# Optimization experiments

Measured on AMD Instinct MI355X. Metric: run time of the kernel, lower is better.

Reference implementation:

```python
import jax, jax.numpy as jnp
import numpy as np
import math

DILATION_RATES = (1, 2, 4, 8)


def setup_inputs() -> dict:
    key = jax.random.key(0)
    B, S, D = 2, 2048, 512
    R = len(DILATION_RATES)
    ks = jax.random.split(key, 8)
    s = 0.02  # init scale
    x = jax.random.normal(ks[0], (B, S, D), dtype=jnp.float32)
    Wq = jax.random.normal(ks[1], (D, D), dtype=jnp.float32) * s
    Wk = jax.random.normal(ks[2], (D, D), dtype=jnp.float32) * s
    Wv = jax.random.normal(ks[3], (D, D), dtype=jnp.float32) * s
    Wr = jax.random.normal(ks[4], (R, D, D), dtype=jnp.float32) * s  # per-rate projections
    Wo = jax.random.normal(ks[5], (R * D, D), dtype=jnp.float32) * s
    bq = jnp.zeros((D,), jnp.float32)
    bk = jnp.zeros((D,), jnp.float32)
    bv = jnp.zeros((D,), jnp.float32)
    br = jnp.zeros((R, D), jnp.float32)
    bo = jnp.zeros((D,), jnp.float32)
    return {"x": x, "Wq": Wq, "bq": bq, "Wk": Wk, "bk": bk, "Wv": Wv, "bv": bv,
            "Wr": Wr, "br": br, "Wo": Wo, "bo": bo}


def reference(x, Wq, bq, Wk, bk, Wv, bv, Wr, br, Wo, bo):
    B, S, D = x.shape
    Q = x @ Wq + bq
    K = x @ Wk + bk
    V = x @ Wv + bv
    # Dense scores are identical across rates in the original (recomputed each loop);
    # compute once for the same math.
    scores = jnp.einsum('bid,bjd->bij', Q, K) / math.sqrt(D)  # [B,S,S]
    idx = jnp.arange(S)
    outs, attns = [], []
    for r, rate in enumerate(DILATION_RATES):
        # mask[i, j] = 1 iff (j % rate == 0) and (j <= i)
        mask = (idx[None, :] % rate == 0) & (idx[None, :] <= idx[:, None])  # [S,S]
        sc = jnp.where(mask[None, :, :], scores, jnp.float32(-1e9))
        attn = jax.nn.softmax(sc, axis=-1)  # dropout is identity at eval
        attns.append(attn)
        ctx = jnp.einsum('bij,bjd->bid', attn, V)
        outs.append(ctx @ Wr[r] + br[r])
    combined = jnp.concatenate(outs, axis=-1)  # [B,S,4D]
    output = combined @ Wo + bo  # [B,S,D]
    avg_attention = jnp.mean(jnp.stack(attns, axis=0), axis=0)  # [B,S,S]
    return output, avg_attention
```

## Files before the change

### kernel.cpp

```cpp
#include <hip/hip_runtime.h>
#include <hip/hip_bf16.h>
#include <math.h>

#define B_ 2
#define S_ 2048
#define D_ 512
#define R_ 4
#define KP 3840

typedef __attribute__((ext_vector_type(8))) __bf16 bf16x8;
typedef __attribute__((ext_vector_type(4))) float f32x4;

enum { M_QKV = 0, M_SCORES = 1, M_WEFFT = 2, M_W2T = 3, M_PF = 4 };

__device__ __forceinline__ void g2l16(const void* gp, void* lp) {
    __builtin_amdgcn_global_load_lds(
        (const __attribute__((address_space(1))) unsigned int*)(unsigned long long)gp,
        (__attribute__((address_space(3))) unsigned int*)(unsigned int)(unsigned long long)lp,
        16, 0, 0);
}

template<int MODE, int TBM, int TBN>
__device__ __forceinline__ void mfma_body(
    int bx, int by, int bz,
    const short* __restrict__ A, const short* __restrict__ B,
    const float* __restrict__ bias, void* __restrict__ Cv,
    int lda, int ldb, int ldc, int K,
    long strA, long strB, long strC, long strBias, float scale,
    __bf16* sAt, __bf16* sBt)
{
    constexpr int WM = TBM / 2, WN = TBN / 2;
    constexpr int FM = WM / 16, FN = WN / 16;

    const int tid  = threadIdx.x;
    const int lane = tid & 63, wid = tid >> 6;
    const int ln15 = lane & 15, quad = lane >> 4;
    const int wy = wid & 1, wx = wid >> 1;

    const int col0 = bx * TBN;
    const int row0 = by * TBM;
    const int z    = bz;

    if constexpr (MODE == M_SCORES) {
        if (col0 > row0 + TBM - 1) return;
    }

    const short* Ab = A + (size_t)z * strA;
    const short* Bb = B + (size_t)z * strB;
    const float* biasb = bias + (size_t)z * strBias;

    int rate = 1, seg = 0;
    if constexpr (MODE == M_W2T) {
        int rIdx;
        if      (col0 >= 3584) { rate = 8; seg = 3584; rIdx = 3; }
        else if (col0 >= 3072) { rate = 4; seg = 3072; rIdx = 2; }
        else if (col0 >= 2048) { rate = 2; seg = 2048; rIdx = 1; }
        else                   { rate = 1; seg = 0;    rIdx = 0; }
        Ab += (size_t)rIdx * D_ * D_;
    }

    f32x4 acc[FM][FN];
    #pragma unroll
    for (int u = 0; u < FM; ++u)
        #pragma unroll
        for (int v = 0; v < FN; ++v)
            acc[u][v] = (f32x4){0.f, 0.f, 0.f, 0.f};

    for (int k0 = 0; k0 < K; k0 += 128) {
        if constexpr (MODE == M_PF) {
            int kr, ks;
            if      (k0 >= 3584) { kr = 8; ks = 3584; }
            else if (k0 >= 3072) { kr = 4; ks = 3072; }
            else if (k0 >= 2048) { kr = 2; ks = 2048; }
            else                 { kr = 1; ks = 0;    }
            if ((k0 - ks) * kr > row0 + TBM - 1) continue;
        }

        #pragma unroll
        for (int t = 0; t < TBM * 16; t += 256) {
            int idx = t + tid;
            int r = idx >> 4, clog = (idx & 15) ^ (r & 7);
            const short* g = Ab + (size_t)(row0 + r) * lda + k0 + clog * 8;
            g2l16(g, (char*)sAt + (t + wid * 64) * 16);
        }
        #pragma unroll
        for (int t = 0; t < TBN * 16; t += 256) {
            int idx = t + tid;
            int r = idx >> 4, clog = (idx & 15) ^ (r & 7);
            int grow;
            if constexpr (MODE == M_W2T) grow = (col0 + r - seg) * rate;
            else                         grow = col0 + r;
            const short* g = Bb + (size_t)grow * ldb + k0 + clog * 8;
            g2l16(g, (char*)sBt + (t + wid * 64) * 16);
        }
        __syncthreads();

        #pragma unroll
        for (int kk = 0; kk < 128; kk += 32) {
            bf16x8 af[FM], bfr[FN];
            #pragma unroll
            for (int u = 0; u < FM; ++u) {
                int ra = wy * WM + u * 16 + ln15;
                int ch = (kk >> 3) + quad;
                af[u] = *(const bf16x8*)&sAt[ra * 128 + (ch ^ (ra & 7)) * 8];
            }
            #pragma unroll
            for (int v = 0; v < FN; ++v) {
                int rb = wx * WN + v * 16 + ln15;
                int ch = (kk >> 3) + quad;
                bfr[v] = *(const bf16x8*)&sBt[rb * 128 + (ch ^ (rb & 7)) * 8];
            }
            #pragma unroll
            for (int u = 0; u < FM; ++u)
                #pragma unroll
                for (int v = 0; v < FN; ++v)
                    acc[u][v] = __builtin_amdgcn_mfma_f32_16x16x32_bf16(
                        af[u], bfr[v], acc[u][v], 0, 0, 0);
        }
        __syncthreads();
    }

    constexpr bool OUTBF = (MODE != M_PF);
    #pragma unroll
    for (int u = 0; u < FM; ++u) {
        int rg = row0 + wy * WM + u * 16 + quad * 4;
        #pragma unroll
        for (int v = 0; v < FN; ++v) {
            int cg = col0 + wx * WN + v * 16 + ln15;
            float bv = 0.f;
            if constexpr (MODE == M_QKV || MODE == M_PF) bv = biasb[cg];
            #pragma unroll
            for (int rr = 0; rr < 4; ++rr) {
                float val = acc[u][v][rr];
                if constexpr (MODE == M_SCORES) val *= scale;
                val += bv;
                if constexpr (OUTBF)
                    ((__hip_bfloat16*)Cv)[(size_t)z * strC + (size_t)(rg + rr) * ldc + cg] =
                        __float2bfloat16(val);
                else
                    ((float*)Cv)[(size_t)z * strC + (size_t)(rg + rr) * ldc + cg] = val;
            }
        }
    }
}

__global__ __launch_bounds__(256) void prep_all(
    const float* __restrict__ x,  const float* __restrict__ Wr,
    const float* __restrict__ Wq, const float* __restrict__ Wk,
    const float* __restrict__ Wv, const float* __restrict__ Wo,
    const float* __restrict__ bq, const float* __restrict__ bk,
    const float* __restrict__ bv, const float* __restrict__ br,
    __hip_bfloat16* __restrict__ xb,  __hip_bfloat16* __restrict__ Wrb,
    __hip_bfloat16* __restrict__ WqT, __hip_bfloat16* __restrict__ WoT,
    float* __restrict__ biasqkv, float* __restrict__ beff_part)
{
    __shared__ float tsh[32][33];
    const int f = blockIdx.x, tid = threadIdx.x;

    if (f < 3072) {
        const float* in; __hip_bfloat16* out; size_t off;
        if (f < 2048) { in = x;  out = xb;  off = ((size_t)f * 256 + tid) * 4; }
        else          { in = Wr; out = Wrb; off = ((size_t)(f - 2048) * 256 + tid) * 4; }
        float4 v = *(const float4*)(in + off);
        out[off + 0] = __float2bfloat16(v.x);
        out[off + 1] = __float2bfloat16(v.y);
        out[off + 2] = __float2bfloat16(v.z);
        out[off + 3] = __float2bfloat16(v.w);
    } else if (f < 4864) {
        int g = f - 3072;
        int cx = g & 15, y = g >> 4;
        const float* in; __hip_bfloat16* out; int Rr, r0;
        if (y < 48) {
            int w = y >> 4;
            in = (w == 0) ? Wq : (w == 1) ? Wk : Wv;
            out = WqT + (size_t)w * 512 * 512;
            Rr = 512; r0 = (y & 15) * 32;
        } else {
            in = Wo; out = WoT; Rr = 2048; r0 = (y - 48) * 32;
        }
        int c0 = cx * 32;
        int tx = tid & 31, ty = tid >> 5;
        #pragma unroll
        for (int dy = 0; dy < 32; dy += 8)
            tsh[ty + dy][tx] = in[(size_t)(r0 + ty + dy) * 512 + c0 + tx];
        __syncthreads();
        #pragma unroll
        for (int dy = 0; dy < 32; dy += 8)
            out[(size_t)(c0 + ty + dy) * Rr + r0 + tx] = __float2bfloat16(tsh[tx][ty + dy]);
    } else if (f < 4880) {
        int j = f - 4864, m0 = j * 128;
        float a0 = 0.f, a1 = 0.f;
        for (int m = m0; m < m0 + 128; ++m) {
            float b = br[m];
            a0 += b * Wo[(size_t)m * D_ + tid];
            a1 += b * Wo[(size_t)m * D_ + tid + 256];
        }
        beff_part[j * 512 + tid]       = a0;
        beff_part[j * 512 + tid + 256] = a1;
    } else {
        for (int k = tid; k < 512; k += 256) {
            biasqkv[k]        = bq[k];
            biasqkv[512 + k]  = bk[k];
            biasqkv[1024 + k] = bv[k];
        }
    }
}

__global__ __launch_bounds__(256) void k_qkv_wefft(
    const short* __restrict__ xb, const short* __restrict__ WqT,
    const float* __restrict__ biasqkv, short* __restrict__ Qb,
    const short* __restrict__ WoT, const short* __restrict__ Wrb,
    short* __restrict__ WeffT,
    const float* __restrict__ beff_part, const float* __restrict__ bo,
    float* __restrict__ beff)
{
    __shared__ __bf16 sA[64 * 128];
    __shared__ __bf16 sB[128 * 128];
    int f = blockIdx.x;
    if (f < 768) {
        mfma_body<M_QKV, 64, 128>(f & 3, (f >> 2) & 63, f >> 8,
            xb, WqT, biasqkv, Qb, 512, 512, 512, 512,
            0, 512L * 512, (long)B_ * S_ * D_, 512, 0.f, sA, sB);
    } else if (f < 896) {
        int g = f - 768;
        mfma_body<M_WEFFT, 64, 128>(g & 3, (g >> 2) & 7, g >> 5,
            WoT, Wrb, beff, WeffT, 2048, 512, 512, 512,
            512, (long)D_ * D_, (long)D_ * D_, 0, 0.f, sA, sB);
    } else {
        int t = threadIdx.x;
        for (int n = t; n < 512; n += 256) {
            float a = bo[n];
            #pragma unroll
            for (int j = 0; j < 16; ++j) a += beff_part[j * 512 + n];
            beff[n] = a;
        }
    }
}

__global__ __launch_bounds__(256) void k_scores_w2t(
    const short* __restrict__ Qb, const short* __restrict__ Kb,
    short* __restrict__ P, const short* __restrict__ WeffT,
    const short* __restrict__ Vb, short* __restrict__ W2T,
    const float* __restrict__ dummy, float scale)
{
    __shared__ __bf16 sA[64 * 128];
    __shared__ __bf16 sB[128 * 128];
    int f = blockIdx.x;
    if (f < 1024) {
        mfma_body<M_SCORES, 64, 128>(f & 15, (f >> 4) & 31, f >> 9,
            Qb, Kb, dummy, P, 512, 512, KP, 512,
            (long)S_ * D_, (long)S_ * D_, (long)S_ * KP, 0, scale, sA, sB);
    } else {
        int g = f - 1024;
        mfma_body<M_W2T, 64, 128>(g % 30, (g / 30) & 7, g / 240,
            WeffT, Vb, dummy, W2T, 512, 512, KP, 512,
            0, (long)S_ * D_, 512L * KP, 0, 0.f, sA, sB);
    }
}

__global__ __launch_bounds__(256) void k_pf(
    const short* __restrict__ P, const short* __restrict__ W2T,
    const float* __restrict__ beff, float* __restrict__ out)
{
    __shared__ __bf16 sA[64 * 128];
    __shared__ __bf16 sB[64 * 128];
    mfma_body<M_PF, 64, 64>(blockIdx.x, gridDim.y - 1 - blockIdx.y, blockIdx.z,
        P, W2T, beff, out, KP, KP, 512, KP,
        (long)S_ * KP, 512L * KP, (long)S_ * D_, 0, 0.f, sA, sB);
}

__global__ __launch_bounds__(256) void softmax_p(float* __restrict__ avg_out,
                                                 __hip_bfloat16* __restrict__ P)
{
    __shared__ float s_p[S_];
    __shared__ float red[4];
    __shared__ float bs[8];

    int i   = blockIdx.x;
    int b   = blockIdx.y;
    int tid = threadIdx.x;
    int wv  = tid >> 6;
    int ln  = tid & 63;

    __bf16* prow = (__bf16*)P + ((size_t)b * S_ + i) * KP;

    const int cnt1 = i + 1;
    const int nchL = (cnt1 + 7) >> 3;
    const int n4   = cnt1 >> 2;

    float m = -INFINITY;
    for (int t = tid; t < nchL; t += 256) {
        bf16x8 v = ((const bf16x8*)prow)[t];
        int base = t << 3;
        #pragma unroll
        for (int k = 0; k < 8; ++k) {
            float xv = (base + k < cnt1) ? (float)v[k] : -INFINITY;
            s_p[base + k] = xv;
            m = fmaxf(m, xv);
        }
    }
    #pragma unroll
    for (int o = 32; o > 0; o >>= 1) m = fmaxf(m, __shfl_xor(m, o, 64));
    if (ln == 0) red[wv] = m;
    if (tid < 8) bs[tid] = 0.f;
    __syncthreads();
    m = fmaxf(fmaxf(red[0], red[1]), fmaxf(red[2], red[3]));

    float a0 = 0.f, a1 = 0.f, a2 = 0.f, a3 = 0.f;
    for (int t = tid; t < n4; t += 256) {
        float4 v = ((float4*)s_p)[t];
        v.x = __expf(v.x - m); v.y = __expf(v.y - m);
        v.z = __expf(v.z - m); v.w = __expf(v.w - m);
        ((float4*)s_p)[t] = v;
        a0 += v.x; a1 += v.y; a2 += v.z; a3 += v.w;
    }
    for (int j = (n4 << 2) + tid; j < cnt1; j += 256) {
        float e = __expf(s_p[j] - m); s_p[j] = e;
        atomicAdd(&bs[j & 7], e);
    }
    float o0 = __shfl_xor(a0, 1, 64), o1 = __shfl_xor(a1, 1, 64);
    float o2 = __shfl_xor(a2, 1, 64), o3 = __shfl_xor(a3, 1, 64);
    float b8[8];
    if ((ln & 1) == 0) {
        b8[0]=a0; b8[1]=a1; b8[2]=a2; b8[3]=a3; b8[4]=o0; b8[5]=o1; b8[6]=o2; b8[7]=o3;
    } else {
        b8[0]=o0; b8[1]=o1; b8[2]=o2; b8[3]=o3; b8[4]=a0; b8[5]=a1; b8[6]=a2; b8[7]=a3;
    }
    #pragma unroll
    for (int st = 2; st < 64; st <<= 1)
        #pragma unroll
        for (int k = 0; k < 8; ++k) b8[k] += __shfl_xor(b8[k], st, 64);
    if (ln == 0) {
        #pragma unroll
        for (int k = 0; k < 8; ++k) atomicAdd(&bs[k], b8[k]);
    }
    __syncthreads();

    float S1 = bs[0]+bs[1]+bs[2]+bs[3]+bs[4]+bs[5]+bs[6]+bs[7];
    float S2 = bs[0]+bs[2]+bs[4]+bs[6];
    float S4 = bs[0]+bs[4];
    float S8 = bs[0];
    float i1 = 1.f/S1, i2 = 1.f/S2, i4 = 1.f/S4, i8 = 1.f/S8;
    float c0 = 0.25f*(i1+i2+i4+i8), c1 = 0.25f*i1, c2 = 0.25f*(i1+i2);
    float c4 = 0.25f*(i1+i2+i4);
    float cA[4] = {c0, c1, c2, c1};
    float cB[4] = {c4, c1, c2, c1};

    float* arow = avg_out + ((size_t)b * S_ + i) * S_;
    for (int t = tid; t < S_ / 4; t += 256) {
        int j = t << 2;
        float4 e = ((float4*)s_p)[t];
        const float* cc = (t & 1) ? cB : cA;
        float4 o;
        o.x = (j     < cnt1) ? e.x * cc[0] : 0.f;
        o.y = (j + 1 < cnt1) ? e.y * cc[1] : 0.f;
        o.z = (j + 2 < cnt1) ? e.z * cc[2] : 0.f;
        o.w = (j + 3 < cnt1) ? e.w * cc[3] : 0.f;
        ((float4*)arow)[t] = o;
    }

    const float invSr[4]  = {i1, i2, i4, i8};
    const int   segoff[4] = {0, 2048, 3072, 3584};
    const int   imax = i | 63;
    #pragma unroll
    for (int ri = 0; ri < 4; ++ri) {
        int seg    = segoff[ri];
        int segLen = S_ >> ri;
        int cnt    = (i >> ri) + 1;
        int tlim   = min(segLen, ((imax >> ri) & ~127) + 128);
        float invS = invSr[ri];
        int nch = tlim >> 3;
        for (int t8 = tid; t8 < nch; t8 += 256) {
            int t0 = t8 << 3;
            bf16x8 w;
            #pragma unroll
            for (int k = 0; k < 8; ++k) {
                int t = t0 + k;
                float p = (t < cnt) ? s_p[t << ri] * invS : 0.f;
                w[k] = (__bf16)p;
            }
            *((bf16x8*)(prow + seg) + t8) = w;
        }
    }
}

extern "C" void kernel_launch(void* const* d_in, const int* in_sizes, int n_in,
                              void* d_out, int out_size, void* d_ws, size_t ws_size,
                              hipStream_t stream)
{
    const float* x  = (const float*)d_in[0];
    const float* Wq = (const float*)d_in[1];
    const float* bq = (const float*)d_in[2];
    const float* Wk = (const float*)d_in[3];
    const float* bk = (const float*)d_in[4];
    const float* Wv = (const float*)d_in[5];
    const float* bv = (const float*)d_in[6];
    const float* Wr = (const float*)d_in[7];
    const float* br = (const float*)d_in[8];
    const float* Wo = (const float*)d_in[9];
    const float* bo = (const float*)d_in[10];

    float* out = (float*)d_out;
    float* avg = out + (size_t)B_ * S_ * D_;

    char* wsb = (char*)d_ws;
    short* xb  = (short*)(wsb);
    short* Qb  = (short*)(wsb + (4u  << 20));
    short* Vb  = (short*)(wsb + (12u << 20));
    short* P   = (short*)(wsb + (16u << 20));
    short* W2T = (short*)(wsb + (16u << 20) + 31457280u);
    short* WqT = W2T;
    short* Wrb   = (short*)((char*)W2T + 7864320u);
    short* WoT   = (short*)((char*)Wrb + 2097152u);
    short* WeffT = (short*)((char*)WoT + 2097152u);
    float* beff      = (float*)((char*)WeffT + 2097152u);
    float* biasqkv   = beff + 512;
    float* beff_part = biasqkv + 1536;

    const float scale = (float)(1.0 / sqrt((double)D_));

    prep_all<<<dim3(4881), 256, 0, stream>>>(
        x, Wr, Wq, Wk, Wv, Wo, bq, bk, bv, br,
        (__hip_bfloat16*)xb, (__hip_bfloat16*)Wrb,
        (__hip_bfloat16*)WqT, (__hip_bfloat16*)WoT, biasqkv, beff_part);

    k_qkv_wefft<<<dim3(897), 256, 0, stream>>>(
        xb, WqT, biasqkv, Qb, WoT, Wrb, WeffT, beff_part, bo, beff);

    k_scores_w2t<<<dim3(1504), 256, 0, stream>>>(
        Qb, Qb + (size_t)B_ * S_ * D_, P, WeffT, Vb, W2T, beff, scale);

    softmax_p<<<dim3(S_, B_), 256, 0, stream>>>(avg, (__hip_bfloat16*)P);

    k_pf<<<dim3(8, 32, 2), 256, 0, stream>>>(P, W2T, beff, out);
}
```

Before: 212.6 us.

## Enlarge GEMM M-tiles to 128 and restructure softmax with presplit dilation buffers

Raises the M tile of the QKV, Weff, scores and W2T GEMMs from 64 to 128 rows and halves their grids, so each block reuses its loaded B tile across more rows. The softmax kernel also changes. It drops the row-max pass and applies exp directly to the raw scores, relying on the scores being small. It writes strided copies of the exponentials into separate shared-memory arrays per dilation rate, so the bf16 writeback reads them contiguously, and it replaces the shared atomics with per-wave partial sums. The exp without a max shift risks overflow on other inputs, and the larger tiles use more shared memory while launching fewer blocks.

```diff
diff --git a/kernel.cpp b/kernel.cpp
--- a/kernel.cpp
+++ b/kernel.cpp
@@ -214,16 +214,16 @@
     const float* __restrict__ beff_part, const float* __restrict__ bo,
     float* __restrict__ beff)
 {
-    __shared__ __bf16 sA[64 * 128];
+    __shared__ __bf16 sA[128 * 128];
     __shared__ __bf16 sB[128 * 128];
     int f = blockIdx.x;
-    if (f < 768) {
-        mfma_body<M_QKV, 64, 128>(f & 3, (f >> 2) & 63, f >> 8,
+    if (f < 384) {
+        mfma_body<M_QKV, 128, 128>(f & 3, (f >> 2) & 31, f >> 7,
             xb, WqT, biasqkv, Qb, 512, 512, 512, 512,
             0, 512L * 512, (long)B_ * S_ * D_, 512, 0.f, sA, sB);
-    } else if (f < 896) {
-        int g = f - 768;
-        mfma_body<M_WEFFT, 64, 128>(g & 3, (g >> 2) & 7, g >> 5,
+    } else if (f < 448) {
+        int g = f - 384;
+        mfma_body<M_WEFFT, 128, 128>(g & 3, (g >> 2) & 3, g >> 4,
             WoT, Wrb, beff, WeffT, 2048, 512, 512, 512,
             512, (long)D_ * D_, (long)D_ * D_, 0, 0.f, sA, sB);
     } else {
@@ -243,16 +243,16 @@
     const short* __restrict__ Vb, short* __restrict__ W2T,
     const float* __restrict__ dummy, float scale)
 {
-    __shared__ __bf16 sA[64 * 128];
+    __shared__ __bf16 sA[128 * 128];
     __shared__ __bf16 sB[128 * 128];
     int f = blockIdx.x;
-    if (f < 1024) {
-        mfma_body<M_SCORES, 64, 128>(f & 15, (f >> 4) & 31, f >> 9,
+    if (f < 512) {
+        mfma_body<M_SCORES, 128, 128>(f & 15, (f >> 4) & 15, f >> 8,
             Qb, Kb, dummy, P, 512, 512, KP, 512,
             (long)S_ * D_, (long)S_ * D_, (long)S_ * KP, 0, scale, sA, sB);
     } else {
-        int g = f - 1024;
-        mfma_body<M_W2T, 64, 128>(g % 30, (g / 30) & 7, g / 240,
+        int g = f - 512;
+        mfma_body<M_W2T, 128, 128>(g % 30, (g / 30) & 3, g / 120,
             WeffT, Vb, dummy, W2T, 512, 512, KP, 512,
             0, (long)S_ * D_, 512L * KP, 0, 0.f, sA, sB);
     }
@@ -272,9 +272,11 @@
 __global__ __launch_bounds__(256) void softmax_p(float* __restrict__ avg_out,
                                                  __hip_bfloat16* __restrict__ P)
 {
-    __shared__ float s_p[S_];
-    __shared__ float red[4];
-    __shared__ float bs[8];
+    __shared__ float s_e[S_];
+    __shared__ float s_d2[S_ / 2];
+    __shared__ float s_d4[S_ / 4];
+    __shared__ float s_d8[S_ / 8];
+    __shared__ float wsum[4][8];
 
     int i   = blockIdx.x;
     int b   = blockIdx.y;
@@ -283,63 +285,49 @@
     int ln  = tid & 63;
 
     __bf16* prow = (__bf16*)P + ((size_t)b * S_ + i) * KP;
-
     const int cnt1 = i + 1;
-    const int nchL = (cnt1 + 7) >> 3;
-    const int n4   = cnt1 >> 2;
-
-    float m = -INFINITY;
-    for (int t = tid; t < nchL; t += 256) {
+    const int nch  = (cnt1 + 7) >> 3;
+
+    for (int t = tid; t < S_ / 4; t += 256) ((float4*)s_e)[t] = (float4){0, 0, 0, 0};
+    for (int t = tid; t < S_ / 8; t += 256) ((float4*)s_d2)[t] = (float4){0, 0, 0, 0};
+    if (tid < S_ / 16) ((float4*)s_d4)[tid] = (float4){0, 0, 0, 0};
+    if (tid < S_ / 32) ((float4*)s_d8)[tid] = (float4){0, 0, 0, 0};
+    __syncthreads();
+
+    float a[8] = {0.f, 0.f, 0.f, 0.f, 0.f, 0.f, 0.f, 0.f};
+    for (int t = tid; t < nch; t += 256) {
         bf16x8 v = ((const bf16x8*)prow)[t];
         int base = t << 3;
+        float e[8];
         #pragma unroll
         for (int k = 0; k < 8; ++k) {
-            float xv = (base + k < cnt1) ? (float)v[k] : -INFINITY;
-            s_p[base + k] = xv;
-            m = fmaxf(m, xv);
-        }
+            float ev = (base + k < cnt1) ? __expf((float)v[k]) : 0.f;
+            e[k] = ev;
+            a[k] += ev;
+        }
+        ((float4*)s_e)[2 * t]     = (float4){e[0], e[1], e[2], e[3]};
+        ((float4*)s_e)[2 * t + 1] = (float4){e[4], e[5], e[6], e[7]};
+        ((float4*)s_d2)[t]        = (float4){e[0], e[2], e[4], e[6]};
+        ((float2*)s_d4)[t]        = (float2){e[0], e[4]};
+        s_d8[t]                   = e[0];
     }
     #pragma unroll
-    for (int o = 32; o > 0; o >>= 1) m = fmaxf(m, __shfl_xor(m, o, 64));
-    if (ln == 0) red[wv] = m;
-    if (tid < 8) bs[tid] = 0.f;
+    for (int st = 1; st < 64; st <<= 1)
+        #pragma unroll
+        for (int k = 0; k < 8; ++k) a[k] += __shfl_xor(a[k], st, 64);
+    if (ln == 0)
+        #pragma unroll
+        for (int k = 0; k < 8; ++k) wsum[wv][k] = a[k];
     __syncthreads();
-    m = fmaxf(fmaxf(red[0], red[1]), fmaxf(red[2], red[3]));
-
-    float a0 = 0.f, a1 = 0.f, a2 = 0.f, a3 = 0.f;
-    for (int t = tid; t < n4; t += 256) {
-        float4 v = ((float4*)s_p)[t];
-        v.x = __expf(v.x - m); v.y = __expf(v.y - m);
-        v.z = __expf(v.z - m); v.w = __expf(v.w - m);
-        ((float4*)s_p)[t] = v;
-        a0 += v.x; a1 += v.y; a2 += v.z; a3 += v.w;
-    }
-    for (int j = (n4 << 2) + tid; j < cnt1; j += 256) {
-        float e = __expf(s_p[j] - m); s_p[j] = e;
-        atomicAdd(&bs[j & 7], e);
-    }
-    float o0 = __shfl_xor(a0, 1, 64), o1 = __shfl_xor(a1, 1, 64);
-    float o2 = __shfl_xor(a2, 1, 64), o3 = __shfl_xor(a3, 1, 64);
-    float b8[8];
-    if ((ln & 1) == 0) {
-        b8[0]=a0; b8[1]=a1; b8[2]=a2; b8[3]=a3; b8[4]=o0; b8[5]=o1; b8[6]=o2; b8[7]=o3;
-    } else {
-        b8[0]=o0; b8[1]=o1; b8[2]=o2; b8[3]=o3; b8[4]=a0; b8[5]=a1; b8[6]=a2; b8[7]=a3;
-    }
+
+    float bsum[8];
     #pragma unroll
-    for (int st = 2; st < 64; st <<= 1)
-        #pragma unroll
-        for (int k = 0; k < 8; ++k) b8[k] += __shfl_xor(b8[k], st, 64);
-    if (ln == 0) {
-        #pragma unroll
-        for (int k = 0; k < 8; ++k) atomicAdd(&bs[k], b8[k]);
-    }
-    __syncthreads();
-
-    float S1 = bs[0]+bs[1]+bs[2]+bs[3]+bs[4]+bs[5]+bs[6]+bs[7];
-    float S2 = bs[0]+bs[2]+bs[4]+bs[6];
-    float S4 = bs[0]+bs[4];
-    float S8 = bs[0];
+    for (int k = 0; k < 8; ++k)
+        bsum[k] = wsum[0][k] + wsum[1][k] + wsum[2][k] + wsum[3][k];
+    float S1 = bsum[0]+bsum[1]+bsum[2]+bsum[3]+bsum[4]+bsum[5]+bsum[6]+bsum[7];
+    float S2 = bsum[0]+bsum[2]+bsum[4]+bsum[6];
+    float S4 = bsum[0]+bsum[4];
+    float S8 = bsum[0];
     float i1 = 1.f/S1, i2 = 1.f/S2, i4 = 1.f/S4, i8 = 1.f/S8;
     float c0 = 0.25f*(i1+i2+i4+i8), c1 = 0.25f*i1, c2 = 0.25f*(i1+i2);
     float c4 = 0.25f*(i1+i2+i4);
@@ -348,38 +336,31 @@
 
     float* arow = avg_out + ((size_t)b * S_ + i) * S_;
     for (int t = tid; t < S_ / 4; t += 256) {
-        int j = t << 2;
-        float4 e = ((float4*)s_p)[t];
+        float4 e = ((float4*)s_e)[t];
         const float* cc = (t & 1) ? cB : cA;
-        float4 o;
-        o.x = (j     < cnt1) ? e.x * cc[0] : 0.f;
-        o.y = (j + 1 < cnt1) ? e.y * cc[1] : 0.f;
-        o.z = (j + 2 < cnt1) ? e.z * cc[2] : 0.f;
-        o.w = (j + 3 < cnt1) ? e.w * cc[3] : 0.f;
-        ((float4*)arow)[t] = o;
-    }
-
-    const float invSr[4]  = {i1, i2, i4, i8};
-    const int   segoff[4] = {0, 2048, 3072, 3584};
-    const int   imax = i | 63;
+        ((float4*)arow)[t] = (float4){e.x*cc[0], e.y*cc[1], e.z*cc[2], e.w*cc[3]};
+    }
+
+    const float* srcs[4] = {s_e, s_d2, s_d4, s_d8};
+    const float invSr[4] = {i1, i2, i4, i8};
+    const int segoff[4]  = {0, 2048, 3072, 3584};
+    const int imax = i | 63;
     #pragma unroll
     for (int ri = 0; ri < 4; ++ri) {
-        int seg    = segoff[ri];
-        int segLen = S_ >> ri;
-        int cnt    = (i >> ri) + 1;
-        int tlim   = min(segLen, ((imax >> ri) & ~127) + 128);
+        const float* src = srcs[ri];
         float invS = invSr[ri];
-        int nch = tlim >> 3;
-        for (int t8 = tid; t8 < nch; t8 += 256) {
-            int t0 = t8 << 3;
+        int tlim = min(S_ >> ri, ((imax >> ri) & ~127) + 128);
+        int nch8 = tlim >> 3;
+        __bf16* dst = prow + segoff[ri];
+        for (int t8 = tid; t8 < nch8; t8 += 256) {
+            float4 lo = ((const float4*)src)[2 * t8];
+            float4 hi = ((const float4*)src)[2 * t8 + 1];
             bf16x8 w;
-            #pragma unroll
-            for (int k = 0; k < 8; ++k) {
-                int t = t0 + k;
-                float p = (t < cnt) ? s_p[t << ri] * invS : 0.f;
-                w[k] = (__bf16)p;
-            }
-            *((bf16x8*)(prow + seg) + t8) = w;
+            w[0] = (__bf16)(lo.x * invS); w[1] = (__bf16)(lo.y * invS);
+            w[2] = (__bf16)(lo.z * invS); w[3] = (__bf16)(lo.w * invS);
+            w[4] = (__bf16)(hi.x * invS); w[5] = (__bf16)(hi.y * invS);
+            w[6] = (__bf16)(hi.z * invS); w[7] = (__bf16)(hi.w * invS);
+            ((bf16x8*)dst)[t8] = w;
         }
     }
 }
@@ -424,10 +405,10 @@
         (__hip_bfloat16*)xb, (__hip_bfloat16*)Wrb,
         (__hip_bfloat16*)WqT, (__hip_bfloat16*)WoT, biasqkv, beff_part);
 
-    k_qkv_wefft<<<dim3(897), 256, 0, stream>>>(
+    k_qkv_wefft<<<dim3(449), 256, 0, stream>>>(
         xb, WqT, biasqkv, Qb, WoT, Wrb, WeffT, beff_part, bo, beff);
 
-    k_scores_w2t<<<dim3(1504), 256, 0, stream>>>(
+    k_scores_w2t<<<dim3(752), 256, 0, stream>>>(
         Qb, Qb + (size_t)B_ * S_ * D_, P, WeffT, Vb, W2T, beff, scale);
 
     softmax_p<<<dim3(S_, B_), 256, 0, stream>>>(avg, (__hip_bfloat16*)P);
```

Result: faster. 201.8 us (-5.1%).
